# Optimization experiments

Hardware: AMD Instinct MI355X
Metric: run time of the kernel (lower is better)

## Reference

```python
import jax, jax.numpy as jnp
import numpy as np

BN_EPS = 1e-5

def _haar_details(x):
    # pywt.dwt2(x, 'haar') details for even H, W.
    # Block [[p, q], [r, s]] with p = x[2i,2j], q = x[2i,2j+1], r = x[2i+1,2j], s = x[2i+1,2j+1].
    # cH ('da'): detail along rows, approx along cols; cV ('ad'); cD ('dd').
    B, C, H, W = x.shape
    xb = x.reshape(B, C, H // 2, 2, W // 2, 2)
    p = xb[:, :, :, 0, :, 0]
    q = xb[:, :, :, 0, :, 1]
    r = xb[:, :, :, 1, :, 0]
    s = xb[:, :, :, 1, :, 1]
    cH = (p + q - r - s) * 0.5
    cV = (p - q + r - s) * 0.5
    cD = (p - q - r + s) * 0.5
    return cH, cV, cD

def setup_inputs() -> dict:
    key = jax.random.key(0)
    k1, k2 = jax.random.split(key)
    B, C, H, W = 8, 256, 128, 128
    x = jax.random.normal(k1, (B, C, H, W), dtype=jnp.float32)
    conv_w = jax.random.normal(k2, (C, 4 * C), dtype=jnp.float32) * (1.0 / np.sqrt(4 * C))
    gamma = jnp.ones((C,), dtype=jnp.float32)
    beta = jnp.zeros((C,), dtype=jnp.float32)
    return {"x": x, "conv_w": conv_w, "gamma": gamma, "beta": beta}

def reference(x, conv_w, gamma, beta):
    B, C, H, W = x.shape
    # Original detaches the wavelet branch (CPU numpy path) -> stop_gradient.
    xs = jax.lax.stop_gradient(x)
    cH, cV, cD = _haar_details(xs)
    # Bilinear upsample to (H, W); jax.image.resize bilinear == torch align_corners=False.
    up = lambda t: jax.image.resize(t, (B, C, H, W), method="bilinear")
    enhanced = jnp.concatenate([x, up(cH), up(cV), up(cD)], axis=1)  # [B, 4C, H, W]
    # 1x1 conv, no bias.
    y = jnp.einsum("bchw,oc->bohw", enhanced, conv_w)  # [B, C, H, W]
    # BatchNorm2d, training-mode (batch statistics, biased variance).
    mean = jnp.mean(y, axis=(0, 2, 3), keepdims=True)
    var = jnp.mean((y - mean) ** 2, axis=(0, 2, 3), keepdims=True)
    y_hat = (y - mean) * jax.lax.rsqrt(var + BN_EPS)
    out = jax.nn.relu(y_hat * gamma[None, :, None, None] + beta[None, :, None, None])
    return out
```

## Files before the change

### kernel.cpp

```cpp
#include <hip/hip_runtime.h>
#include <hip/hip_bf16.h>

typedef __bf16 bf16;
typedef __bf16 bf16x4 __attribute__((ext_vector_type(4)));
typedef __bf16 bf16x8 __attribute__((ext_vector_type(8)));
typedef float  f32x4  __attribute__((ext_vector_type(4)));

#define AS1 __attribute__((address_space(1)))
#define AS3 __attribute__((address_space(3)))

__device__ __forceinline__ void load16_to_lds(const bf16* g, bf16* l) {
    __builtin_amdgcn_global_load_lds((const AS1 unsigned int*)g,
                                     (AS3 unsigned int*)l, 16, 0, 0);
}

__global__ __launch_bounds__(256) void pass0(const float* __restrict__ x,
                                             const float* __restrict__ cw,
                                             bf16* __restrict__ wb,
                                             bf16* __restrict__ xt,
                                             bf16* __restrict__ cT) {
    __shared__ bf16 tile[64 * 264];
    const int bid = blockIdx.x;
    const int t = threadIdx.x;
    if (bid >= 2048) {
        int idx = ((bid - 2048) * 256 + t) * 4;
        const float4 v = *(const float4*)(cw + idx);
        bf16x4 o; o[0]=(bf16)v.x; o[1]=(bf16)v.y; o[2]=(bf16)v.z; o[3]=(bf16)v.w;
        *(bf16x4*)(wb + idx) = o;
        return;
    }
    const int wt = bid & 3, j = (bid >> 2) & 63, b = bid >> 8;
    const int w0 = wt * 32;

    for (int i = 0; i < 16; ++i) {
        int g = i * 256 + t;
        int c = g >> 4;
        int rem = g & 15;
        int dlt = rem >> 3, w4 = rem & 7;
        const float4 v = *(const float4*)(x +
            ((((size_t)b * 256 + c) * 128 + (2 * j + dlt)) * 128 + w0 + w4 * 4));
        int pos = dlt * 32 + w4 * 4;
        tile[(pos + 0) * 264 + c] = (bf16)v.x;
        tile[(pos + 1) * 264 + c] = (bf16)v.y;
        tile[(pos + 2) * 264 + c] = (bf16)v.z;
        tile[(pos + 3) * 264 + c] = (bf16)v.w;
    }
    __syncthreads();

    for (int i = 0; i < 8; ++i) {
        int q = i * 256 + t;
        int cq = q & 31, pos = q >> 5;
        int dlt = pos >> 5, w = pos & 31;
        bf16x8 v = *(const bf16x8*)&tile[pos * 264 + cq * 8];
        int h = 2 * j + dlt, wg = w0 + w;
        *(bf16x8*)(xt + (((size_t)b * 16384 + h * 128 + wg) * 256 + cq * 8)) = v;
    }

    for (int i = 0; i < 2; ++i) {
        int q = i * 256 + t;
        int cq = q & 31, kc = q >> 5;
        bf16x8 vp = *(const bf16x8*)&tile[(2 * kc) * 264 + cq * 8];
        bf16x8 vq = *(const bf16x8*)&tile[(2 * kc + 1) * 264 + cq * 8];
        bf16x8 vr = *(const bf16x8*)&tile[(32 + 2 * kc) * 264 + cq * 8];
        bf16x8 vs = *(const bf16x8*)&tile[(33 + 2 * kc) * 264 + cq * 8];
        bf16x8 oh, ov, od;
        #pragma unroll
        for (int e = 0; e < 8; ++e) {
            float p = (float)vp[e], qq = (float)vq[e];
            float r = (float)vr[e], s = (float)vs[e];
            oh[e] = (bf16)(0.5f * (p + qq - r - s));
            ov[e] = (bf16)(0.5f * (p - qq + r - s));
            od[e] = (bf16)(0.5f * (p - qq - r + s));
        }
        size_t row = ((size_t)b * 4096 + j * 64 + wt * 16 + kc) * 768;
        *(bf16x8*)(cT + row + 0 * 256 + cq * 8) = oh;
        *(bf16x8*)(cT + row + 1 * 256 + cq * 8) = ov;
        *(bf16x8*)(cT + row + 2 * 256 + cq * 8) = od;
    }
}

__global__ __launch_bounds__(256) void gemm_all(const bf16* __restrict__ W,
                                                const bf16* __restrict__ cT,
                                                const bf16* __restrict__ xt,
                                                bf16* __restrict__ z,
                                                bf16* __restrict__ y1) {
    __shared__ bf16 Wt[128 * 32];
    __shared__ bf16 Xt[128 * 32];
    const int bid = blockIdx.x;
    const bf16* X; bf16* Y; int K, kofs, mshift, m0, o0;
    if (bid < 512) {
        K = 768; kofs = 256; mshift = 12; X = cT; Y = z;
        m0 = (bid & 255) * 128; o0 = (bid >> 8) * 128;
    } else {
        int b1 = bid - 512;
        K = 256; kofs = 0; mshift = 14; X = xt; Y = y1;
        m0 = (b1 & 1023) * 128; o0 = (b1 >> 10) * 128;
    }
    const int t = threadIdx.x;
    const int wave = t >> 6, lane = t & 63;
    const int quad = lane >> 4, l16 = lane & 15;
    const int wo = (wave >> 1) * 64, wm = (wave & 1) * 64;
    const int Mplane = 1 << mshift;
    const int r_in = lane >> 2;
    const int cch = lane & 3;

    f32x4 acc[4][4] = {};

    const bf16* wbase = W + (size_t)o0 * 1024 + kofs;
    const bf16* xbase = X + (size_t)m0 * K;

    for (int kk = 0; kk < K; kk += 32) {
        #pragma unroll
        for (int i = 0; i < 2; ++i) {
            int rblk = wave * 2 + i;
            int row = rblk * 16 + r_in;
            load16_to_lds(wbase + (size_t)row * 1024 + kk + cch * 8,
                          &Wt[rblk * 512 + lane * 8]);
            load16_to_lds(xbase + (size_t)row * K + kk + cch * 8,
                          &Xt[rblk * 512 + lane * 8]);
        }
        __syncthreads();
        bf16x8 af[4], bfr[4];
        #pragma unroll
        for (int i = 0; i < 4; ++i)
            af[i] = *(const bf16x8*)&Wt[(wo + i * 16 + l16) * 32 + quad * 8];
        #pragma unroll
        for (int jj = 0; jj < 4; ++jj)
            bfr[jj] = *(const bf16x8*)&Xt[(wm + jj * 16 + l16) * 32 + quad * 8];
        #pragma unroll
        for (int i = 0; i < 4; ++i)
            #pragma unroll
            for (int jj = 0; jj < 4; ++jj)
                acc[i][jj] = __builtin_amdgcn_mfma_f32_16x16x32_bf16(
                    bfr[jj], af[i], acc[i][jj], 0, 0, 0);
        __syncthreads();
    }

    #pragma unroll
    for (int i = 0; i < 4; ++i) {
        int o = o0 + wo + i * 16 + l16;
        #pragma unroll
        for (int jj = 0; jj < 4; ++jj) {
            int m = m0 + wm + jj * 16 + quad * 4;
            int bb = m >> mshift;
            int mp = m & (Mplane - 1);
            bf16x4 v;
            #pragma unroll
            for (int r = 0; r < 4; ++r) v[r] = (bf16)acc[i][jj][r];
            *(bf16x4*)(Y + ((size_t)bb * 256 + o) * Mplane + mp) = v;
        }
    }
}

__device__ __forceinline__ void load_zplane(const bf16* zp, float* zs, int t) {
    for (int i = 0; i < 2; ++i) {
        int idx = (i * 256 + t) * 8;
        int j = idx >> 6, k = idx & 63;
        bf16x8 v = *(const bf16x8*)(zp + idx);
        #pragma unroll
        for (int e = 0; e < 8; ++e) zs[j * 65 + k + e] = (float)v[e];
    }
}

__device__ __forceinline__ void up8(const float* zs, int base, float* u) {
    int h = base >> 7, w0 = base & 127;
    int j0 = h >> 1;
    int jn = (h & 1) ? min(j0 + 1, 63) : max(j0 - 1, 0);
    int K = w0 >> 1;
    float z0[6], z1[6];
    #pragma unroll
    for (int d = 0; d < 6; ++d) {
        int kc = min(max(K - 1 + d, 0), 63);
        z0[d] = zs[j0 * 65 + kc];
        z1[d] = zs[jn * 65 + kc];
    }
    #pragma unroll
    for (int e = 0; e < 8; ++e) {
        int a = (e >> 1) + 1;
        int bb = (e & 1) ? a + 1 : a - 1;
        u[e] = 0.5625f * z0[a] + 0.1875f * (z0[bb] + z1[a]) + 0.0625f * z1[bb];
    }
}

__global__ __launch_bounds__(256) void stats_k(const bf16* __restrict__ y1,
                                               const bf16* __restrict__ z,
                                               float* __restrict__ stats) {
    __shared__ float zs[64 * 65];
    __shared__ float red[8];
    const int bid = blockIdx.x;
    const int o = bid & 255, b = bid >> 8;
    const int t = threadIdx.x;
    const bf16* zp = z + ((size_t)b * 256 + o) * 4096;
    const bf16* yp = y1 + ((size_t)b * 256 + o) * 16384;
    load_zplane(zp, zs, t);
    __syncthreads();
    float s = 0.f, ss = 0.f;
    for (int i = 0; i < 8; ++i) {
        int base = (i * 256 + t) * 8;
        float u[8];
        up8(zs, base, u);
        bf16x8 yv = *(const bf16x8*)(yp + base);
        #pragma unroll
        for (int e = 0; e < 8; ++e) {
            float y = (float)yv[e] + u[e];
            s += y; ss += y * y;
        }
    }
    #pragma unroll
    for (int off = 32; off > 0; off >>= 1) {
        s += __shfl_down(s, off);
        ss += __shfl_down(ss, off);
    }
    if ((t & 63) == 0) { red[t >> 6] = s; red[4 + (t >> 6)] = ss; }
    __syncthreads();
    if (t == 0) {
        atomicAdd(&stats[o],       red[0] + red[1] + red[2] + red[3]);
        atomicAdd(&stats[256 + o], red[4] + red[5] + red[6] + red[7]);
    }
}

__global__ __launch_bounds__(256) void finalize_k(float* __restrict__ stats,
                                                  const float* __restrict__ gamma,
                                                  const float* __restrict__ beta) {
    int o = threadIdx.x;
    const float n = 131072.f;
    float mean = stats[o] / n;
    float var = stats[256 + o] / n - mean * mean;
    float rstd = rsqrtf(var + 1e-5f);
    float sc = rstd * gamma[o];
    stats[512 + o] = sc;
    stats[768 + o] = beta[o] - mean * sc;
}

__global__ __launch_bounds__(256) void apply_k(const bf16* __restrict__ y1,
                                               const bf16* __restrict__ z,
                                               const float* __restrict__ stats,
                                               float* __restrict__ out) {
    __shared__ float zs[64 * 65];
    const int bid = blockIdx.x;
    const int o = bid & 255, b = bid >> 8;
    const int t = threadIdx.x;
    const bf16* zp = z + ((size_t)b * 256 + o) * 4096;
    const bf16* yp = y1 + ((size_t)b * 256 + o) * 16384;
    float* op = out + ((size_t)b * 256 + o) * 16384;
    const float sc = stats[512 + o], sh = stats[768 + o];
    load_zplane(zp, zs, t);
    __syncthreads();
    for (int i = 0; i < 8; ++i) {
        int base = (i * 256 + t) * 8;
        float u[8];
        up8(zs, base, u);
        bf16x8 yv = *(const bf16x8*)(yp + base);
        float4 o0, o1;
        o0.x = fmaxf(fmaf((float)yv[0] + u[0], sc, sh), 0.f);
        o0.y = fmaxf(fmaf((float)yv[1] + u[1], sc, sh), 0.f);
        o0.z = fmaxf(fmaf((float)yv[2] + u[2], sc, sh), 0.f);
        o0.w = fmaxf(fmaf((float)yv[3] + u[3], sc, sh), 0.f);
        o1.x = fmaxf(fmaf((float)yv[4] + u[4], sc, sh), 0.f);
        o1.y = fmaxf(fmaf((float)yv[5] + u[5], sc, sh), 0.f);
        o1.z = fmaxf(fmaf((float)yv[6] + u[6], sc, sh), 0.f);
        o1.w = fmaxf(fmaf((float)yv[7] + u[7], sc, sh), 0.f);
        *(float4*)(op + base) = o0;
        *(float4*)(op + base + 4) = o1;
    }
}

extern "C" void kernel_launch(void* const* d_in, const int* in_sizes, int n_in,
                              void* d_out, int out_size, void* d_ws, size_t ws_size,
                              hipStream_t stream) {
    const float* x      = (const float*)d_in[0];
    const float* conv_w = (const float*)d_in[1];
    const float* gamma  = (const float*)d_in[2];
    const float* beta   = (const float*)d_in[3];
    float* out = (float*)d_out;

    char* ws = (char*)d_ws;
    bf16*  Wbf   = (bf16*)ws;
    bf16*  xt    = (bf16*)(ws + (512ll << 10));
    bf16*  z     = (bf16*)(ws + (512ll << 10) + (64ll << 20));
    float* stats = (float*)(ws + (512ll << 10) + (80ll << 20));
    bf16*  cT    = (bf16*)(ws + (512ll << 10) + (80ll << 20) + 4096);
    bf16*  y1    = (bf16*)(ws + (512ll << 10) + (128ll << 20) + 4096);

    hipMemsetAsync(stats, 0, 4096, stream);
    pass0<<<2304, 256, 0, stream>>>(x, conv_w, Wbf, xt, cT);
    gemm_all<<<2560, 256, 0, stream>>>(Wbf, cT, xt, z, y1);
    stats_k<<<2048, 256, 0, stream>>>(y1, z, stats);
    finalize_k<<<1, 256, 0, stream>>>(stats, gamma, beta);
    apply_k<<<2048, 256, 0, stream>>>(y1, z, stats, out);
}
```

Baseline: 352.0 us.

## Fuse x-branch GEMM into transpose kernel, drop xt intermediate, read W from global

The transpose/haar kernel now also computes the x-part of the 1x1 conv directly from its LDS tile, using MFMA with weight fragments loaded from global memory, and writes y1. This removes the 16 MB bf16 xt intermediate write and reread. The weight conversion becomes its own small kernel, and the detail GEMM now reads W fragments straight from global instead of staging them in LDS. The cost is that every block rereads W from global/L2 and the fused kernel carries high register pressure at occupancy 2.

```diff
diff --git a/kernel.cpp b/kernel.cpp
--- a/kernel.cpp
+++ b/kernel.cpp
@@ -14,22 +14,22 @@
                                      (AS3 unsigned int*)l, 16, 0, 0);
 }
 
-__global__ __launch_bounds__(256) void pass0(const float* __restrict__ x,
-                                             const float* __restrict__ cw,
-                                             bf16* __restrict__ wb,
-                                             bf16* __restrict__ xt,
-                                             bf16* __restrict__ cT) {
+__global__ __launch_bounds__(256) void prep_w(const float* __restrict__ w,
+                                              bf16* __restrict__ wb) {
+    int idx = (blockIdx.x * 256 + threadIdx.x) * 4;
+    const float4 v = *(const float4*)(w + idx);
+    bf16x4 o; o[0]=(bf16)v.x; o[1]=(bf16)v.y; o[2]=(bf16)v.z; o[3]=(bf16)v.w;
+    *(bf16x4*)(wb + idx) = o;
+}
+
+__global__ __launch_bounds__(256, 2) void fused_x(const float* __restrict__ x,
+                                                  const bf16* __restrict__ W,
+                                                  bf16* __restrict__ cT,
+                                                  bf16* __restrict__ y1) {
     __shared__ bf16 tile[64 * 264];
     const int bid = blockIdx.x;
+    const int wt = bid & 3, j = (bid >> 2) & 63, b = bid >> 8;
     const int t = threadIdx.x;
-    if (bid >= 2048) {
-        int idx = ((bid - 2048) * 256 + t) * 4;
-        const float4 v = *(const float4*)(cw + idx);
-        bf16x4 o; o[0]=(bf16)v.x; o[1]=(bf16)v.y; o[2]=(bf16)v.z; o[3]=(bf16)v.w;
-        *(bf16x4*)(wb + idx) = o;
-        return;
-    }
-    const int wt = bid & 3, j = (bid >> 2) & 63, b = bid >> 8;
     const int w0 = wt * 32;
 
     for (int i = 0; i < 16; ++i) {
@@ -47,15 +47,6 @@
     }
     __syncthreads();
 
-    for (int i = 0; i < 8; ++i) {
-        int q = i * 256 + t;
-        int cq = q & 31, pos = q >> 5;
-        int dlt = pos >> 5, w = pos & 31;
-        bf16x8 v = *(const bf16x8*)&tile[pos * 264 + cq * 8];
-        int h = 2 * j + dlt, wg = w0 + w;
-        *(bf16x8*)(xt + (((size_t)b * 16384 + h * 128 + wg) * 256 + cq * 8)) = v;
-    }
-
     for (int i = 0; i < 2; ++i) {
         int q = i * 256 + t;
         int cq = q & 31, kc = q >> 5;
@@ -77,53 +68,76 @@
         *(bf16x8*)(cT + row + 1 * 256 + cq * 8) = ov;
         *(bf16x8*)(cT + row + 2 * 256 + cq * 8) = od;
     }
-}
-
-__global__ __launch_bounds__(256) void gemm_all(const bf16* __restrict__ W,
-                                                const bf16* __restrict__ cT,
-                                                const bf16* __restrict__ xt,
-                                                bf16* __restrict__ z,
-                                                bf16* __restrict__ y1) {
-    __shared__ bf16 Wt[128 * 32];
+
+    const int wave = t >> 6, lane = t & 63;
+    const int quad = lane >> 4, l16 = lane & 15;
+    const int wo = wave * 64;
+    f32x4 acc[4][4] = {};
+    for (int kk = 0; kk < 256; kk += 32) {
+        bf16x8 xf[4], wf[4];
+        #pragma unroll
+        for (int i = 0; i < 4; ++i)
+            xf[i] = *(const bf16x8*)&tile[(i * 16 + l16) * 264 + kk + quad * 8];
+        #pragma unroll
+        for (int jj = 0; jj < 4; ++jj)
+            wf[jj] = *(const bf16x8*)(W +
+                (size_t)(wo + jj * 16 + l16) * 1024 + kk + quad * 8);
+        #pragma unroll
+        for (int i = 0; i < 4; ++i)
+            #pragma unroll
+            for (int jj = 0; jj < 4; ++jj)
+                acc[i][jj] = __builtin_amdgcn_mfma_f32_16x16x32_bf16(
+                    xf[i], wf[jj], acc[i][jj], 0, 0, 0);
+    }
+
+    #pragma unroll
+    for (int i = 0; i < 4; ++i) {
+        int p = i * 16 + quad * 4;
+        int h = 2 * j + (p >> 5), wc = w0 + (p & 31);
+        #pragma unroll
+        for (int jj = 0; jj < 4; ++jj) {
+            int o = wo + jj * 16 + l16;
+            bf16x4 v;
+            #pragma unroll
+            for (int r = 0; r < 4; ++r) v[r] = (bf16)acc[i][jj][r];
+            *(bf16x4*)(y1 + ((size_t)b * 256 + o) * 16384 + h * 128 + wc) = v;
+        }
+    }
+}
+
+__global__ __launch_bounds__(256) void gemm2(const bf16* __restrict__ W,
+                                             const bf16* __restrict__ cT,
+                                             bf16* __restrict__ z) {
     __shared__ bf16 Xt[128 * 32];
     const int bid = blockIdx.x;
-    const bf16* X; bf16* Y; int K, kofs, mshift, m0, o0;
-    if (bid < 512) {
-        K = 768; kofs = 256; mshift = 12; X = cT; Y = z;
-        m0 = (bid & 255) * 128; o0 = (bid >> 8) * 128;
-    } else {
-        int b1 = bid - 512;
-        K = 256; kofs = 0; mshift = 14; X = xt; Y = y1;
-        m0 = (b1 & 1023) * 128; o0 = (b1 >> 10) * 128;
-    }
+    const int m0 = (bid & 255) * 128, o0 = (bid >> 8) * 128;
     const int t = threadIdx.x;
     const int wave = t >> 6, lane = t & 63;
     const int quad = lane >> 4, l16 = lane & 15;
     const int wo = (wave >> 1) * 64, wm = (wave & 1) * 64;
-    const int Mplane = 1 << mshift;
-    const int r_in = lane >> 2;
-    const int cch = lane & 3;
+    const int r_in = lane >> 2, cch = lane & 3;
 
     f32x4 acc[4][4] = {};
-
-    const bf16* wbase = W + (size_t)o0 * 1024 + kofs;
-    const bf16* xbase = X + (size_t)m0 * K;
-
-    for (int kk = 0; kk < K; kk += 32) {
+    const bf16* wbase = W + (size_t)o0 * 1024 + 256;
+    const bf16* xbase = cT + (size_t)m0 * 768;
+
+    for (int kk = 0; kk < 768; kk += 32) {
+        {
+            int row = wave * 32 + (lane >> 1);
+        }
         #pragma unroll
         for (int i = 0; i < 2; ++i) {
             int rblk = wave * 2 + i;
             int row = rblk * 16 + r_in;
-            load16_to_lds(wbase + (size_t)row * 1024 + kk + cch * 8,
-                          &Wt[rblk * 512 + lane * 8]);
-            load16_to_lds(xbase + (size_t)row * K + kk + cch * 8,
+            load16_to_lds(xbase + (size_t)row * 768 + kk + cch * 8,
                           &Xt[rblk * 512 + lane * 8]);
         }
         __syncthreads();
         bf16x8 af[4], bfr[4];
         #pragma unroll
         for (int i = 0; i < 4; ++i)
-            af[i] = *(const bf16x8*)&Wt[(wo + i * 16 + l16) * 32 + quad * 8];
+            af[i] = *(const bf16x8*)(wbase +
+                (size_t)(wo + i * 16 + l16) * 1024 + kk + quad * 8);
         #pragma unroll
         for (int jj = 0; jj < 4; ++jj)
             bfr[jj] = *(const bf16x8*)&Xt[(wm + jj * 16 + l16) * 32 + quad * 8];
@@ -142,12 +156,11 @@
         #pragma unroll
         for (int jj = 0; jj < 4; ++jj) {
             int m = m0 + wm + jj * 16 + quad * 4;
-            int bb = m >> mshift;
-            int mp = m & (Mplane - 1);
+            int bb = m >> 12, mp = m & 4095;
             bf16x4 v;
             #pragma unroll
             for (int r = 0; r < 4; ++r) v[r] = (bf16)acc[i][jj][r];
-            *(bf16x4*)(Y + ((size_t)bb * 256 + o) * Mplane + mp) = v;
+            *(bf16x4*)(z + ((size_t)bb * 256 + o) * 4096 + mp) = v;
         }
     }
 }
@@ -276,15 +289,15 @@
 
     char* ws = (char*)d_ws;
     bf16*  Wbf   = (bf16*)ws;
-    bf16*  xt    = (bf16*)(ws + (512ll << 10));
-    bf16*  z     = (bf16*)(ws + (512ll << 10) + (64ll << 20));
-    float* stats = (float*)(ws + (512ll << 10) + (80ll << 20));
-    bf16*  cT    = (bf16*)(ws + (512ll << 10) + (80ll << 20) + 4096);
-    bf16*  y1    = (bf16*)(ws + (512ll << 10) + (128ll << 20) + 4096);
+    bf16*  z     = (bf16*)(ws + (512ll << 10));
+    float* stats = (float*)(ws + (512ll << 10) + (16ll << 20));
+    bf16*  cT    = (bf16*)(ws + (512ll << 10) + (16ll << 20) + 4096);
+    bf16*  y1    = (bf16*)(ws + (512ll << 10) + (64ll << 20) + 4096);
 
     hipMemsetAsync(stats, 0, 4096, stream);
-    pass0<<<2304, 256, 0, stream>>>(x, conv_w, Wbf, xt, cT);
-    gemm_all<<<2560, 256, 0, stream>>>(Wbf, cT, xt, z, y1);
+    prep_w<<<256, 256, 0, stream>>>(conv_w, Wbf);
+    fused_x<<<2048, 256, 0, stream>>>(x, Wbf, cT, y1);
+    gemm2<<<512, 256, 0, stream>>>(Wbf, cT, z);
     stats_k<<<2048, 256, 0, stream>>>(y1, z, stats);
     finalize_k<<<1, 256, 0, stream>>>(stats, gamma, beta);
     apply_k<<<2048, 256, 0, stream>>>(y1, z, stats, out);
```

Result: no change. 352.2 us (+0.1%).
